# Kernel tuning notes

Measured on AMD Instinct MI355X. Metric: run time of the kernel, lower is better.

Reference implementation:

```python
import jax, jax.numpy as jnp
import numpy as np

N_NODES = 100000
N_EDGES = 1600000
IN_C, HID_C, OUT_C = 128, 128, 64


def gcn_conv(x, src, dst, W, b, num_nodes):
    # PyG GCNConv: add self-loops, symmetric normalization, linear transform,
    # aggregate source features into targets.
    h = x @ W  # [N, C_out]
    loop = jnp.arange(num_nodes, dtype=src.dtype)
    s = jnp.concatenate([src, loop])
    d = jnp.concatenate([dst, loop])
    deg = jax.ops.segment_sum(jnp.ones_like(d, dtype=h.dtype), d, num_segments=num_nodes)
    inv_sqrt = jnp.where(deg > 0, jax.lax.rsqrt(deg), 0.0)
    norm = inv_sqrt[s] * inv_sqrt[d]  # [E+N]
    msgs = h[s] * norm[:, None]  # gather + scale
    out = jax.ops.segment_sum(msgs, d, num_segments=num_nodes)  # scatter-add
    return out + b


def setup_inputs() -> dict:
    key = jax.random.key(0)
    k1, k2, k3, k4 = jax.random.split(key, 4)
    x = jax.random.normal(k1, (N_NODES, IN_C), dtype=jnp.float32)
    edge_index = jax.random.randint(k2, (2, N_EDGES), 0, N_NODES, dtype=jnp.int64)
    W1 = jax.random.normal(k3, (IN_C, HID_C), dtype=jnp.float32) * (1.0 / np.sqrt(IN_C))
    b1 = jnp.zeros((HID_C,), dtype=jnp.float32)
    W2 = jax.random.normal(k4, (HID_C, OUT_C), dtype=jnp.float32) * (1.0 / np.sqrt(HID_C))
    b2 = jnp.zeros((OUT_C,), dtype=jnp.float32)
    return {"x": x, "edge_index": edge_index, "W1": W1, "b1": b1, "W2": W2, "b2": b2}


def reference(x, edge_index, W1, b1, W2, b2):
    num_nodes = x.shape[0]
    src, dst = edge_index[0], edge_index[1]  # PyG flow: source -> target
    h = gcn_conv(x, src, dst, W1, b1, num_nodes)
    h = jax.nn.relu(h)  # dropout is identity in eval mode
    out = gcn_conv(h, src, dst, W2, b2, num_nodes)
    return out
```

## Files before the change

### kernel.cpp

```cpp
#include <hip/hip_runtime.h>

#define IN_C 128
#define HID_C 128
#define OUT_C 64

#define BSPAN 256
#define BCAP  5120
#define NBMAX 512
#define ACHUNK 4096

typedef unsigned int uint32;
typedef unsigned short ushort16;


__device__ __forceinline__ ushort16 f2bf(float f) {
    union { float f; uint32 u; } v; v.f = f;
    uint32 r = v.u + 0x7FFFu + ((v.u >> 16) & 1u);
    return (ushort16)(r >> 16);
}

__device__ __forceinline__ void unpack2(uint32 u, float& f0, float& f1) {
    union { uint32 x; float f; } a, b;
    a.x = u << 16;
    b.x = u & 0xFFFF0000u;
    f0 = a.f; f1 = b.f;
}


__launch_bounds__(256)
__global__ void bin_edges_kernel(const int* __restrict__ src, const int* __restrict__ dst,
                                 int* __restrict__ bucketCur, uint32* __restrict__ binned,
                                 int E, int nbuck) {
    __shared__ int hist[NBMAX];
    __shared__ int base[NBMAX];
    __shared__ int rank[NBMAX];
    const int tid = threadIdx.x;
    const int e0  = blockIdx.x * ACHUNK;

    for (int i = tid; i < NBMAX; i += 256) { hist[i] = 0; rank[i] = 0; }
    __syncthreads();

    int d[16], s[16];
#pragma unroll
    for (int j = 0; j < 16; j++) {
        int e = e0 + j * 256 + tid;
        if (e < E) {
            d[j] = dst[e];
            s[j] = src[e];
            atomicAdd(&hist[d[j] >> 8], 1);
        } else d[j] = -1;
    }
    __syncthreads();

    for (int b = tid; b < nbuck; b += 256) {
        int h = hist[b];
        base[b] = h ? atomicAdd(&bucketCur[b], h) : 0;
    }
    __syncthreads();

#pragma unroll
    for (int j = 0; j < 16; j++) {
        if (d[j] >= 0) {
            int b = d[j] >> 8;
            int r = atomicAdd(&rank[b], 1);
            int pos = base[b] + r;
            if (pos < BCAP)
                binned[(size_t)b * BCAP + pos] =
                    ((uint32)(d[j] & 255) << 17) | (uint32)s[j];
        }
    }
}


__launch_bounds__(256)
__global__ void bucket_csr_kernel(const uint32* __restrict__ binned,
                                  const int* __restrict__ bucketCur,
                                  int* __restrict__ csr_src, int* __restrict__ rowbeg,
                                  int* __restrict__ rowend, float* __restrict__ inv, int N) {
    __shared__ int cnt[BSPAN];
    __shared__ int scn[BSPAN];
    __shared__ int cur[BSPAN];
    const int b   = blockIdx.x;
    const int tid = threadIdx.x;
    const int n0  = b * BSPAN;
    const int ne  = min(bucketCur[b], BCAP);
    const uint32* bp = binned + (size_t)b * BCAP;

    cnt[tid] = 0;
    __syncthreads();
    for (int i = tid; i < ne; i += 256)
        atomicAdd(&cnt[bp[i] >> 17], 1);
    __syncthreads();

    int v = cnt[tid];
    scn[tid] = v;
    __syncthreads();
    for (int off = 1; off < 256; off <<= 1) {
        int u = (tid >= off) ? scn[tid - off] : 0;
        __syncthreads();
        scn[tid] += u;
        __syncthreads();
    }
    int excl = scn[tid] - v;
    cur[tid] = excl;

    int n = n0 + tid;
    if (n < N) {
        int gb = b * BCAP + excl;
        rowbeg[n] = gb;
        rowend[n] = gb + v;
        inv[n] = rsqrtf((float)(v + 1));
    }
    __syncthreads();

    for (int i = tid; i < ne; i += 256) {
        uint32 e = bp[i];
        int r = atomicAdd(&cur[e >> 17], 1);
        csr_src[(size_t)b * BCAP + r] = (int)(e & 0x1FFFFu);
    }
}


template <int C>
__launch_bounds__(256)
__global__ void gemm_tile(const float* __restrict__ X, const float* __restrict__ W,
                          const float* __restrict__ inv, ushort16* __restrict__ outb, int N) {
    constexpr int K   = 128;
    constexpr int KC  = 32;
    constexpr int M   = 64;
    constexpr int CPT = C / 16;
    __shared__ float Xs[M][36];
    __shared__ float Ws[KC][C];

    const int tid = threadIdx.x;
    const int tx  = tid & 15;
    const int ty  = tid >> 4;
    const int c0  = tx * CPT;
    const int r0  = ty * 4;
    const int row0 = blockIdx.x * M;

    float acc[4][CPT];
#pragma unroll
    for (int i = 0; i < 4; i++)
#pragma unroll
        for (int c = 0; c < CPT; c++) acc[i][c] = 0.f;

    for (int kc = 0; kc < K; kc += KC) {
        __syncthreads();
#pragma unroll
        for (int t = 0; t < (M * KC / 4) / 256; t++) {
            int f   = tid + t * 256;
            int r   = f >> 3;
            int k4  = (f & 7) * 4;
            int row = row0 + r;
            float4 v = make_float4(0.f, 0.f, 0.f, 0.f);
            if (row < N) v = *(const float4*)(X + (size_t)row * K + kc + k4);
            *(float4*)&Xs[r][k4] = v;
        }
#pragma unroll
        for (int t = 0; t < (KC * C / 4) / 256; t++) {
            int f  = tid + t * 256;
            int kk = f / (C / 4);
            int c4 = (f % (C / 4)) * 4;
            *(float4*)&Ws[kk][c4] = *(const float4*)(W + (size_t)(kc + kk) * C + c4);
        }
        __syncthreads();

#pragma unroll
        for (int k4 = 0; k4 < KC; k4 += 4) {
            float xr[4][4];
#pragma unroll
            for (int i = 0; i < 4; i++)
                *(float4*)xr[i] = *(const float4*)&Xs[r0 + i][k4];
#pragma unroll
            for (int kk = 0; kk < 4; kk++) {
#pragma unroll
                for (int cv = 0; cv < CPT / 4; cv++) {
                    float4 wv = *(const float4*)&Ws[k4 + kk][c0 + cv * 4];
#pragma unroll
                    for (int i = 0; i < 4; i++) {
                        acc[i][cv * 4 + 0] = fmaf(xr[i][kk], wv.x, acc[i][cv * 4 + 0]);
                        acc[i][cv * 4 + 1] = fmaf(xr[i][kk], wv.y, acc[i][cv * 4 + 1]);
                        acc[i][cv * 4 + 2] = fmaf(xr[i][kk], wv.z, acc[i][cv * 4 + 2]);
                        acc[i][cv * 4 + 3] = fmaf(xr[i][kk], wv.w, acc[i][cv * 4 + 3]);
                    }
                }
            }
        }
    }

#pragma unroll
    for (int i = 0; i < 4; i++) {
        int row = row0 + r0 + i;
        if (row >= N) continue;
        float iv = inv[row];
        ushort16 tmp[CPT];
#pragma unroll
        for (int c = 0; c < CPT; c++) tmp[c] = f2bf(acc[i][c] * iv);
        ushort16* dst = outb + (size_t)row * C + c0;
        if (CPT == 8) {
            *(uint4*)dst = *(const uint4*)tmp;
        } else {
            *(uint2*)dst = *(const uint2*)tmp;
        }
    }
}


template <int C, bool RELU>
__launch_bounds__(256)
__global__ void gather_agg_bf16(const int* __restrict__ rowbeg, const int* __restrict__ rowend,
                                const int* __restrict__ csr_src,
                                const ushort16* __restrict__ hsb, const float* __restrict__ inv,
                                const float* __restrict__ b, float* __restrict__ out, int N) {
    constexpr int TPN = C / 8;
    constexpr int NPB = 256 / TPN;
    int n    = blockIdx.x * NPB + threadIdx.x / TPN;
    int lane = threadIdx.x % TPN;
    if (n >= N) return;
    int c8 = lane * 8;

    float acc[8];
    {
        uint4 raw = *(const uint4*)(hsb + (size_t)n * C + c8);
        unpack2(raw.x, acc[0], acc[1]);
        unpack2(raw.y, acc[2], acc[3]);
        unpack2(raw.z, acc[4], acc[5]);
        unpack2(raw.w, acc[6], acc[7]);
    }

    int beg = rowbeg[n];
    int end = rowend[n];
    int i = beg;
    for (; i + 2 <= end; i += 2) {
        int s0 = csr_src[i];
        int s1 = csr_src[i + 1];
        uint4 r0 = *(const uint4*)(hsb + (size_t)s0 * C + c8);
        uint4 r1 = *(const uint4*)(hsb + (size_t)s1 * C + c8);
        float f0, f1;
        unpack2(r0.x, f0, f1); acc[0] += f0; acc[1] += f1;
        unpack2(r0.y, f0, f1); acc[2] += f0; acc[3] += f1;
        unpack2(r0.z, f0, f1); acc[4] += f0; acc[5] += f1;
        unpack2(r0.w, f0, f1); acc[6] += f0; acc[7] += f1;
        unpack2(r1.x, f0, f1); acc[0] += f0; acc[1] += f1;
        unpack2(r1.y, f0, f1); acc[2] += f0; acc[3] += f1;
        unpack2(r1.z, f0, f1); acc[4] += f0; acc[5] += f1;
        unpack2(r1.w, f0, f1); acc[6] += f0; acc[7] += f1;
    }
    if (i < end) {
        int s0 = csr_src[i];
        uint4 r0 = *(const uint4*)(hsb + (size_t)s0 * C + c8);
        float f0, f1;
        unpack2(r0.x, f0, f1); acc[0] += f0; acc[1] += f1;
        unpack2(r0.y, f0, f1); acc[2] += f0; acc[3] += f1;
        unpack2(r0.z, f0, f1); acc[4] += f0; acc[5] += f1;
        unpack2(r0.w, f0, f1); acc[6] += f0; acc[7] += f1;
    }

    float iv = inv[n];
    float4 b0 = *(const float4*)(b + c8);
    float4 b1 = *(const float4*)(b + c8 + 4);
    float r[8];
    r[0] = fmaf(iv, acc[0], b0.x); r[1] = fmaf(iv, acc[1], b0.y);
    r[2] = fmaf(iv, acc[2], b0.z); r[3] = fmaf(iv, acc[3], b0.w);
    r[4] = fmaf(iv, acc[4], b1.x); r[5] = fmaf(iv, acc[5], b1.y);
    r[6] = fmaf(iv, acc[6], b1.z); r[7] = fmaf(iv, acc[7], b1.w);
    if (RELU) {
#pragma unroll
        for (int j = 0; j < 8; j++) r[j] = fmaxf(r[j], 0.f);
    }
    float* po = out + (size_t)n * C + c8;
    *(float4*)(po)     = make_float4(r[0], r[1], r[2], r[3]);
    *(float4*)(po + 4) = make_float4(r[4], r[5], r[6], r[7]);
}

extern "C" void kernel_launch(void* const* d_in, const int* in_sizes, int n_in,
                              void* d_out, int out_size, void* d_ws, size_t ws_size,
                              hipStream_t stream) {
    const float* x  = (const float*)d_in[0];
    const int*   ei = (const int*)d_in[1];
    const float* W1 = (const float*)d_in[2];
    const float* b1 = (const float*)d_in[3];
    const float* W2 = (const float*)d_in[4];
    const float* b2 = (const float*)d_in[5];
    float* out = (float*)d_out;

    const int N = in_sizes[0] / IN_C;
    const int E = in_sizes[1] / 2;
    const int* src = ei;
    const int* dst = ei + E;
    const int nbuck = (N + BSPAN - 1) / BSPAN;

    char* ws = (char*)d_ws;
    auto align_up = [](size_t v) { return (v + 1023) & ~(size_t)1023; };
    size_t off = 0;
    int*      bucketCur = (int*)(ws + off);      off += align_up((size_t)nbuck * sizeof(int));
    float*    inv       = (float*)(ws + off);    off += align_up((size_t)N * sizeof(float));
    int*      rowbeg    = (int*)(ws + off);      off += align_up((size_t)N * sizeof(int));
    int*      rowend    = (int*)(ws + off);      off += align_up((size_t)N * sizeof(int));
    uint32*   binned    = (uint32*)(ws + off);   off += align_up((size_t)nbuck * BCAP * sizeof(uint32));
    int*      csrs      = (int*)(ws + off);      off += align_up((size_t)nbuck * BCAP * sizeof(int));
    ushort16* hs1b      = (ushort16*)(ws + off); off += align_up((size_t)N * HID_C * sizeof(ushort16));
    float*    h1post    = (float*)(ws + off);    off += align_up((size_t)N * HID_C * sizeof(float));
    ushort16* hs2b      = (ushort16*)(ws + off); off += align_up((size_t)N * OUT_C * sizeof(ushort16));

    hipMemsetAsync(bucketCur, 0, (size_t)nbuck * sizeof(int), stream);
    bin_edges_kernel<<<(E + ACHUNK - 1) / ACHUNK, 256, 0, stream>>>(
        src, dst, bucketCur, binned, E, nbuck);
    bucket_csr_kernel<<<nbuck, 256, 0, stream>>>(
        binned, bucketCur, csrs, rowbeg, rowend, inv, N);

    gemm_tile<HID_C><<<(N + 63) / 64, 256, 0, stream>>>(x, W1, inv, hs1b, N);
    {
        constexpr int NPB = 256 / (HID_C / 8);
        gather_agg_bf16<HID_C, true><<<(N + NPB - 1) / NPB, 256, 0, stream>>>(
            rowbeg, rowend, csrs, hs1b, inv, b1, h1post, N);
    }

    gemm_tile<OUT_C><<<(N + 63) / 64, 256, 0, stream>>>(h1post, W2, inv, hs2b, N);
    {
        constexpr int NPB = 256 / (OUT_C / 8);
        gather_agg_bf16<OUT_C, false><<<(N + NPB - 1) / NPB, 256, 0, stream>>>(
            rowbeg, rowend, csrs, hs2b, inv, b2, out, N);
    }
}
```

Baseline: 306.2 us.

## Replace FP32 tiled GEMMs with FP16 MFMA GEMMs and store hidden activations in FP16

Replaces the scalar-FMA shared-memory GEMM with a matrix-core kernel built on mfma_f32_16x16x32_f16. The weights are pre-swizzled into FP16 fragment layout by a small prep kernel, and the input rows are converted to FP16 as they are loaded into shared memory. The first aggregation now writes the ReLU hidden layer in FP16 rather than FP32, which halves its write traffic and the second GEMM's read traffic. The cost is lower precision in the GEMM inputs and the hidden layer, plus two extra tiny launches for weight prep.

```diff
diff --git a/kernel.cpp b/kernel.cpp
--- a/kernel.cpp
+++ b/kernel.cpp
@@ -11,6 +11,9 @@
 
 typedef unsigned int uint32;
 typedef unsigned short ushort16;
+typedef _Float16 f16;
+typedef f16   f16x8 __attribute__((ext_vector_type(8)));
+typedef float f32x4 __attribute__((ext_vector_type(4)));
 
 
 __device__ __forceinline__ ushort16 f2bf(float f) {
@@ -122,97 +125,130 @@
 
 
 template <int C>
+__global__ void wprep_kernel(const float* __restrict__ W, f16* __restrict__ Wf) {
+    constexpr int NCT = C / 16;
+    int t = blockIdx.x * 256 + threadIdx.x;
+    if (t >= 4 * NCT * 64) return;
+    int lane = t & 63;
+    int ctkc = t >> 6;
+    int ct = ctkc % NCT, kc = ctkc / NCT;
+    int kbase = kc * 32 + (lane >> 4) * 8;
+    int col   = ct * 16 + (lane & 15);
+    f16 v[8];
+#pragma unroll
+    for (int j = 0; j < 8; j++) v[j] = (f16)W[(size_t)(kbase + j) * C + col];
+    *(uint4*)(Wf + (size_t)t * 8) = *(const uint4*)v;
+}
+
+
+template <int C, bool AF16>
 __launch_bounds__(256)
-__global__ void gemm_tile(const float* __restrict__ X, const float* __restrict__ W,
+__global__ void mfma_gemm(const void* __restrict__ Xv, const f16* __restrict__ Wf,
                           const float* __restrict__ inv, ushort16* __restrict__ outb, int N) {
-    constexpr int K   = 128;
-    constexpr int KC  = 32;
-    constexpr int M   = 64;
-    constexpr int CPT = C / 16;
-    __shared__ float Xs[M][36];
-    __shared__ float Ws[KC][C];
-
-    const int tid = threadIdx.x;
-    const int tx  = tid & 15;
-    const int ty  = tid >> 4;
-    const int c0  = tx * CPT;
-    const int r0  = ty * 4;
-    const int row0 = blockIdx.x * M;
-
-    float acc[4][CPT];
-#pragma unroll
-    for (int i = 0; i < 4; i++)
-#pragma unroll
-        for (int c = 0; c < CPT; c++) acc[i][c] = 0.f;
-
-    for (int kc = 0; kc < K; kc += KC) {
-        __syncthreads();
-#pragma unroll
-        for (int t = 0; t < (M * KC / 4) / 256; t++) {
-            int f   = tid + t * 256;
-            int r   = f >> 3;
-            int k4  = (f & 7) * 4;
-            int row = row0 + r;
-            float4 v = make_float4(0.f, 0.f, 0.f, 0.f);
-            if (row < N) v = *(const float4*)(X + (size_t)row * K + kc + k4);
-            *(float4*)&Xs[r][k4] = v;
-        }
-#pragma unroll
-        for (int t = 0; t < (KC * C / 4) / 256; t++) {
-            int f  = tid + t * 256;
-            int kk = f / (C / 4);
-            int c4 = (f % (C / 4)) * 4;
-            *(float4*)&Ws[kk][c4] = *(const float4*)(W + (size_t)(kc + kk) * C + c4);
-        }
-        __syncthreads();
-
-#pragma unroll
-        for (int k4 = 0; k4 < KC; k4 += 4) {
-            float xr[4][4];
-#pragma unroll
-            for (int i = 0; i < 4; i++)
-                *(float4*)xr[i] = *(const float4*)&Xs[r0 + i][k4];
-#pragma unroll
-            for (int kk = 0; kk < 4; kk++) {
-#pragma unroll
-                for (int cv = 0; cv < CPT / 4; cv++) {
-                    float4 wv = *(const float4*)&Ws[k4 + kk][c0 + cv * 4];
-#pragma unroll
-                    for (int i = 0; i < 4; i++) {
-                        acc[i][cv * 4 + 0] = fmaf(xr[i][kk], wv.x, acc[i][cv * 4 + 0]);
-                        acc[i][cv * 4 + 1] = fmaf(xr[i][kk], wv.y, acc[i][cv * 4 + 1]);
-                        acc[i][cv * 4 + 2] = fmaf(xr[i][kk], wv.z, acc[i][cv * 4 + 2]);
-                        acc[i][cv * 4 + 3] = fmaf(xr[i][kk], wv.w, acc[i][cv * 4 + 3]);
-                    }
-                }
+    constexpr int NCT = C / 16;
+    __shared__ __align__(16) f16 As[4 * 4 * 64 * 8];
+    __shared__ __align__(16) f16 Bs[4 * NCT * 64 * 8];
+
+    const int tid  = threadIdx.x;
+    const int lane = tid & 63;
+    const int w    = tid >> 6;
+    const int row0 = blockIdx.x * 64;
+
+    {
+        constexpr int TOT = 4 * NCT * 64 * 8;
+        const uint4* src = (const uint4*)Wf;
+        uint4* dst = (uint4*)Bs;
+#pragma unroll
+        for (int i = 0; i < TOT / 8 / 256; i++)
+            dst[tid + i * 256] = src[tid + i * 256];
+    }
+
+    {
+        int r   = tid >> 2;
+        int seg = tid & 3;
+        int row = row0 + r;
+        int ws_ = r >> 4;
+        int r15 = r & 15;
+        if (!AF16) {
+            const float* X = (const float*)Xv;
+#pragma unroll
+            for (int i = 0; i < 8; i++) {
+                int k = seg * 32 + i * 4;
+                float4 v = make_float4(0.f, 0.f, 0.f, 0.f);
+                if (row < N) v = *(const float4*)(X + (size_t)row * 128 + k);
+                int q = (k >> 3) & 3, j0 = k & 7;
+                f16 h[4] = {(f16)v.x, (f16)v.y, (f16)v.z, (f16)v.w};
+                int slot = ((seg * 4 + ws_) * 64 + (q * 16 + r15)) * 8 + j0;
+                *(uint2*)(As + slot) = *(const uint2*)h;
             }
-        }
-    }
-
-#pragma unroll
-    for (int i = 0; i < 4; i++) {
-        int row = row0 + r0 + i;
-        if (row >= N) continue;
-        float iv = inv[row];
-        ushort16 tmp[CPT];
-#pragma unroll
-        for (int c = 0; c < CPT; c++) tmp[c] = f2bf(acc[i][c] * iv);
-        ushort16* dst = outb + (size_t)row * C + c0;
-        if (CPT == 8) {
-            *(uint4*)dst = *(const uint4*)tmp;
         } else {
-            *(uint2*)dst = *(const uint2*)tmp;
-        }
-    }
-}
-
-
-template <int C, bool RELU>
+            const f16* X = (const f16*)Xv;
+#pragma unroll
+            for (int i = 0; i < 4; i++) {
+                int k = seg * 32 + i * 8;
+                uint4 v = make_uint4(0, 0, 0, 0);
+                if (row < N) v = *(const uint4*)(X + (size_t)row * 128 + k);
+                int q = (k >> 3) & 3;
+                int slot = ((seg * 4 + ws_) * 64 + (q * 16 + r15)) * 8;
+                *(uint4*)(As + slot) = v;
+            }
+        }
+    }
+    __syncthreads();
+
+    f32x4 acc[NCT];
+#pragma unroll
+    for (int c = 0; c < NCT; c++) acc[c] = (f32x4){0.f, 0.f, 0.f, 0.f};
+
+#pragma unroll
+    for (int kc = 0; kc < 4; kc++) {
+        f16x8 a = *(const f16x8*)&As[((kc * 4 + w) * 64 + lane) * 8];
+#pragma unroll
+        for (int ct = 0; ct < NCT; ct++) {
+            f16x8 b = *(const f16x8*)&Bs[((kc * NCT + ct) * 64 + lane) * 8];
+            acc[ct] = __builtin_amdgcn_mfma_f32_16x16x32_f16(a, b, acc[ct], 0, 0, 0);
+        }
+    }
+
+    __syncthreads();
+    ushort16* Ds = (ushort16*)As;
+    const int q = lane >> 4;
+    float iv[4];
+#pragma unroll
+    for (int reg = 0; reg < 4; reg++) {
+        int row = row0 + w * 16 + q * 4 + reg;
+        iv[reg] = (row < N) ? inv[row] : 0.f;
+    }
+#pragma unroll
+    for (int ct = 0; ct < NCT; ct++) {
+#pragma unroll
+        for (int reg = 0; reg < 4; reg++) {
+            int r = w * 16 + q * 4 + reg;
+            Ds[r * C + ct * 16 + (lane & 15)] = f2bf(acc[ct][reg] * iv[reg]);
+        }
+    }
+    __syncthreads();
+    {
+        int r  = tid >> 2;
+        int row = row0 + r;
+        if (row < N) {
+            constexpr int SPT = C / 4;
+            int c0 = (tid & 3) * SPT;
+            const uint4* s = (const uint4*)&Ds[r * C + c0];
+            uint4* d = (uint4*)(outb + (size_t)row * C + c0);
+#pragma unroll
+            for (int i = 0; i < SPT / 8; i++) d[i] = s[i];
+        }
+    }
+}
+
+
+template <int C, bool RELU, bool F16OUT>
 __launch_bounds__(256)
 __global__ void gather_agg_bf16(const int* __restrict__ rowbeg, const int* __restrict__ rowend,
                                 const int* __restrict__ csr_src,
                                 const ushort16* __restrict__ hsb, const float* __restrict__ inv,
-                                const float* __restrict__ b, float* __restrict__ out, int N) {
+                                const float* __restrict__ b, void* __restrict__ outv, int N) {
     constexpr int TPN = C / 8;
     constexpr int NPB = 256 / TPN;
     int n    = blockIdx.x * NPB + threadIdx.x / TPN;
@@ -269,9 +305,16 @@
 #pragma unroll
         for (int j = 0; j < 8; j++) r[j] = fmaxf(r[j], 0.f);
     }
-    float* po = out + (size_t)n * C + c8;
-    *(float4*)(po)     = make_float4(r[0], r[1], r[2], r[3]);
-    *(float4*)(po + 4) = make_float4(r[4], r[5], r[6], r[7]);
+    if (F16OUT) {
+        f16 o[8];
+#pragma unroll
+        for (int j = 0; j < 8; j++) o[j] = (f16)r[j];
+        *(uint4*)((f16*)outv + (size_t)n * C + c8) = *(const uint4*)o;
+    } else {
+        float* po = (float*)outv + (size_t)n * C + c8;
+        *(float4*)(po)     = make_float4(r[0], r[1], r[2], r[3]);
+        *(float4*)(po + 4) = make_float4(r[4], r[5], r[6], r[7]);
+    }
 }
 
 extern "C" void kernel_launch(void* const* d_in, const int* in_sizes, int n_in,
@@ -300,27 +343,31 @@
     int*      rowend    = (int*)(ws + off);      off += align_up((size_t)N * sizeof(int));
     uint32*   binned    = (uint32*)(ws + off);   off += align_up((size_t)nbuck * BCAP * sizeof(uint32));
     int*      csrs      = (int*)(ws + off);      off += align_up((size_t)nbuck * BCAP * sizeof(int));
+    f16*      Wf1       = (f16*)(ws + off);      off += align_up((size_t)4 * (HID_C/16) * 64 * 8 * sizeof(f16));
+    f16*      Wf2       = (f16*)(ws + off);      off += align_up((size_t)4 * (OUT_C/16) * 64 * 8 * sizeof(f16));
     ushort16* hs1b      = (ushort16*)(ws + off); off += align_up((size_t)N * HID_C * sizeof(ushort16));
-    float*    h1post    = (float*)(ws + off);    off += align_up((size_t)N * HID_C * sizeof(float));
+    f16*      h1post    = (f16*)(ws + off);      off += align_up((size_t)N * HID_C * sizeof(f16));
     ushort16* hs2b      = (ushort16*)(ws + off); off += align_up((size_t)N * OUT_C * sizeof(ushort16));
 
     hipMemsetAsync(bucketCur, 0, (size_t)nbuck * sizeof(int), stream);
+    wprep_kernel<HID_C><<<(4 * (HID_C/16) * 64 + 255) / 256, 256, 0, stream>>>(W1, Wf1);
+    wprep_kernel<OUT_C><<<(4 * (OUT_C/16) * 64 + 255) / 256, 256, 0, stream>>>(W2, Wf2);
     bin_edges_kernel<<<(E + ACHUNK - 1) / ACHUNK, 256, 0, stream>>>(
         src, dst, bucketCur, binned, E, nbuck);
     bucket_csr_kernel<<<nbuck, 256, 0, stream>>>(
         binned, bucketCur, csrs, rowbeg, rowend, inv, N);
 
-    gemm_tile<HID_C><<<(N + 63) / 64, 256, 0, stream>>>(x, W1, inv, hs1b, N);
+    mfma_gemm<HID_C, false><<<(N + 63) / 64, 256, 0, stream>>>(x, Wf1, inv, hs1b, N);
     {
         constexpr int NPB = 256 / (HID_C / 8);
-        gather_agg_bf16<HID_C, true><<<(N + NPB - 1) / NPB, 256, 0, stream>>>(
+        gather_agg_bf16<HID_C, true, true><<<(N + NPB - 1) / NPB, 256, 0, stream>>>(
             rowbeg, rowend, csrs, hs1b, inv, b1, h1post, N);
     }
 
-    gemm_tile<OUT_C><<<(N + 63) / 64, 256, 0, stream>>>(h1post, W2, inv, hs2b, N);
+    mfma_gemm<OUT_C, true><<<(N + 63) / 64, 256, 0, stream>>>(h1post, Wf2, inv, hs2b, N);
     {
         constexpr int NPB = 256 / (OUT_C / 8);
-        gather_agg_bf16<OUT_C, false><<<(N + NPB - 1) / NPB, 256, 0, stream>>>(
+        gather_agg_bf16<OUT_C, false, false><<<(N + NPB - 1) / NPB, 256, 0, stream>>>(
             rowbeg, rowend, csrs, hs2b, inv, b2, out, N);
     }
 }
```

Result: faster. 271.6 us (-11.3%).
